# Kernel tuning notes

Measured on AMD Instinct MI355X. Metric: run time of the kernel, lower is better.

Reference implementation:

```python
import jax, jax.numpy as jnp
import numpy as np

D_MODEL = 1024

def setup_inputs() -> dict:
    key = jax.random.key(0)
    ks = jax.random.split(key, 5)
    s = 1.0 / np.sqrt(D_MODEL)  # torch Linear default init scale-ish
    x = jax.random.normal(ks[0], (4, 2048, D_MODEL), dtype=jnp.float32)
    Wq = jax.random.normal(ks[1], (D_MODEL, D_MODEL), dtype=jnp.float32) * s
    Wk = jax.random.normal(ks[2], (D_MODEL, D_MODEL), dtype=jnp.float32) * s
    Wv = jax.random.normal(ks[3], (D_MODEL, D_MODEL), dtype=jnp.float32) * s
    Wo = jax.random.normal(ks[4], (D_MODEL, D_MODEL), dtype=jnp.float32) * s
    z = jnp.zeros((D_MODEL,), dtype=jnp.float32)
    return {"x": x, "Wq": Wq, "bq": z, "Wk": Wk, "bk": z, "Wv": Wv, "bv": z, "Wo": Wo, "bo": z}

def reference(x, Wq, bq, Wk, bk, Wv, bv, Wo, bo):
    # x: (B, S, D). Single-head causal attention, dropout in eval mode (identity).
    B, S, D = x.shape
    Q = jnp.einsum('bsd,ed->bse', x, Wq) + bq
    K = jnp.einsum('bsd,ed->bse', x, Wk) + bk
    V = jnp.einsum('bsd,ed->bse', x, Wv) + bv
    scores = jnp.einsum('bqd,bkd->bqk', Q, K) / jnp.sqrt(jnp.float32(D))
    causal = jnp.tril(jnp.ones((S, S), dtype=bool))  # (S, S)
    scores = jnp.where(causal, scores, -jnp.inf)
    weights = jax.nn.softmax(scores, axis=-1)
    attended = jnp.einsum('bqk,bkd->bqd', weights, V)
    out = jnp.einsum('bsd,ed->bse', attended, Wo) + bo
    return out
```

## Files before the change

kernel.cpp:

```cpp
#include <hip/hip_runtime.h>
#include <cstdint>
#include <cstddef>


#define D_MODEL 1024
#define SEQ     2048
#define BATCH   4

typedef unsigned short u16;
typedef __bf16 bf16_t;
typedef bf16_t bf16x8 __attribute__((ext_vector_type(8)));
typedef float  f32x4  __attribute__((ext_vector_type(4)));
typedef u16    u16x4  __attribute__((ext_vector_type(4)));

__device__ __forceinline__ u16 f2bf(float x) {
  union { float f; uint32_t u; } v; v.f = x;
  uint32_t r = v.u + 0x7fffu + ((v.u >> 16) & 1u);
  return (u16)(r >> 16);
}
__device__ __forceinline__ float bf2f(u16 h) {
  union { uint32_t u; float f; } v; v.u = (uint32_t)h << 16;
  return v.f;
}

__device__ __forceinline__ void gload_lds16(const u16* g, u16* l) {
  __builtin_amdgcn_global_load_lds((__attribute__((address_space(1))) void*)g,
                                   (__attribute__((address_space(3))) void*)l,
                                   16, 0, 0);
}

__device__ __forceinline__ void gemm_core(const u16* __restrict__ Ablk,
                                          const u16* __restrict__ Bblk,
                                          int lda, int ldb, int ksteps32,
                                          u16* As, u16* Bs,
                                          f32x4 acc[4][4]) {
  const int tid  = threadIdx.x;
  const int lane = tid & 63;
  const int wave = tid >> 6;
  const int wr = (wave >> 1) * 64, wc = (wave & 1) * 64;
  const int frow = lane & 15, kc = lane >> 4;
  const int ch0 = tid, ch1 = 256 + tid;
  const int m0 = ch0 >> 2, k80 = (((ch0 & 3) ^ ((m0 >> 1) & 3))) * 8;
  const int m1 = ch1 >> 2, k81 = (((ch1 & 3) ^ ((m1 >> 1) & 3))) * 8;
  int aoff[4], boff[4];
#pragma unroll
  for (int i = 0; i < 4; ++i) {
    const int ra = wr + i * 16 + frow;
    aoff[i] = (ra * 4 + (kc ^ ((ra >> 1) & 3))) * 8;
    const int rb = wc + i * 16 + frow;
    boff[i] = (rb * 4 + (kc ^ ((rb >> 1) & 3))) * 8;
  }
  for (int kt = 0; kt < ksteps32; ++kt) {
    __syncthreads();
    const int kb = kt * 32;
    gload_lds16(Ablk + (size_t)m0 * lda + kb + k80, As + ch0 * 8);
    gload_lds16(Ablk + (size_t)m1 * lda + kb + k81, As + ch1 * 8);
    gload_lds16(Bblk + (size_t)m0 * ldb + kb + k80, Bs + ch0 * 8);
    gload_lds16(Bblk + (size_t)m1 * ldb + kb + k81, Bs + ch1 * 8);
    asm volatile("s_waitcnt vmcnt(0)" ::: "memory");
    __syncthreads();

    bf16x8 af[4], bf[4];
#pragma unroll
    for (int i = 0; i < 4; ++i) af[i] = *(const bf16x8*)(As + aoff[i]);
#pragma unroll
    for (int j = 0; j < 4; ++j) bf[j] = *(const bf16x8*)(Bs + boff[j]);
#pragma unroll
    for (int i = 0; i < 4; ++i)
#pragma unroll
      for (int j = 0; j < 4; ++j)
        acc[i][j] = __builtin_amdgcn_mfma_f32_16x16x32_bf16(af[i], bf[j], acc[i][j], 0, 0, 0);
  }
}

__global__ __launch_bounds__(256) void cvt_kernel(const float4* __restrict__ x,
                                                  const float4* __restrict__ wq,
                                                  const float4* __restrict__ wk,
                                                  const float4* __restrict__ wv,
                                                  const float4* __restrict__ wo,
                                                  u16* __restrict__ dst) {
  const int i = blockIdx.x * 256 + threadIdx.x;
  float4 v;
  if (i < 2097152) {
    v = x[i];
  } else {
    const int j = i - 2097152;
    const int w = j >> 18;
    const float4* s = (w == 0) ? wq : (w == 1) ? wk : (w == 2) ? wv : wo;
    v = s[j & 262143];
  }
  u16x4 o = {f2bf(v.x), f2bf(v.y), f2bf(v.z), f2bf(v.w)};
  *(u16x4*)(dst + (size_t)i * 4) = o;
}

__global__ void transposeW_kernel(const u16* __restrict__ src, u16* __restrict__ dst) {
  __shared__ u16 tile[32][33];
  const int r0 = blockIdx.x * 32, c0 = blockIdx.y * 32;
  const int tx = threadIdx.x, ty = threadIdx.y;
#pragma unroll
  for (int r = 0; r < 4; ++r)
    tile[ty + r * 8][tx] = src[(size_t)(r0 + ty + r * 8) * D_MODEL + c0 + tx];
  __syncthreads();
#pragma unroll
  for (int r = 0; r < 4; ++r)
    dst[(size_t)(c0 + ty + r * 8) * D_MODEL + r0 + tx] = tile[tx][ty + r * 8];
}

__global__ __launch_bounds__(256) void stageA_kernel(
    const u16* __restrict__ xb,
    const u16* __restrict__ WqB, const u16* __restrict__ WkB,
    const u16* __restrict__ WoB, const u16* __restrict__ WvT,
    const float* __restrict__ Wo32, const float* __restrict__ bv,
    const float* __restrict__ bq, const float* __restrict__ bk,
    u16* __restrict__ Qb, u16* __restrict__ Kb,
    u16* __restrict__ Wp, float* __restrict__ bp) {
  __shared__ __align__(16) u16 As[4096];
  __shared__ __align__(16) u16 Bs[4096];
  const int blk = blockIdx.x;
  const int lane = threadIdx.x & 63, wave = threadIdx.x >> 6;
  const int wr = (wave >> 1) * 64, wc = (wave & 1) * 64;
  const int cl = lane & 15, rl = (lane >> 4) * 4;

  if (blk < 64) {
    const int f0 = (blk >> 3) * 128, e0 = (blk & 7) * 128;
    f32x4 acc[4][4] = {};
    gemm_core(WoB + (size_t)f0 * D_MODEL, WvT + (size_t)e0 * D_MODEL,
              D_MODEL, D_MODEL, 32, As, Bs, acc);
#pragma unroll
    for (int j = 0; j < 4; ++j) {
      const int col = e0 + wc + j * 16 + cl;
#pragma unroll
      for (int i = 0; i < 4; ++i)
#pragma unroll
        for (int r = 0; r < 4; ++r) {
          const int row = f0 + wr + i * 16 + rl + r;
          Wp[(size_t)row * D_MODEL + col] = f2bf(acc[i][j][r]);
        }
    }
  } else if (blk < 80) {
    const int f = (blk - 64) * 64 + (threadIdx.x >> 2);
    const int dq = threadIdx.x & 3;
    const float* row = Wo32 + (size_t)f * D_MODEL + dq * 256;
    const float* bvq = bv + dq * 256;
    float s = 0.f;
#pragma unroll 8
    for (int i = 0; i < 256; ++i) s += row[i] * bvq[i];
    s += __shfl_xor(s, 1);
    s += __shfl_xor(s, 2);
    if (dq == 0) bp[f] = s;
  } else {
    const int v = blk - 80;
    const int c = v & 7, s = v >> 3;
    const int row0 = (c * 8 + (s >> 4)) * 128;
    const int cz = s & 15;
    const int z = cz >> 3;
    const int col0 = (cz & 7) * 128;
    const u16*   W    = z ? WkB : WqB;
    const float* bias = z ? bk : bq;
    u16*         out  = z ? Kb : Qb;
    f32x4 acc[4][4] = {};
    gemm_core(xb + (size_t)row0 * D_MODEL, W + (size_t)col0 * D_MODEL,
              D_MODEL, D_MODEL, 32, As, Bs, acc);
#pragma unroll
    for (int j = 0; j < 4; ++j) {
      const int col = col0 + wc + j * 16 + cl;
      const float bb = bias[col];
#pragma unroll
      for (int i = 0; i < 4; ++i)
#pragma unroll
        for (int r = 0; r < 4; ++r) {
          const int row = row0 + wr + i * 16 + rl + r;
          out[(size_t)row * D_MODEL + col] = f2bf(acc[i][j][r] + bb);
        }
    }
  }
}

__global__ __launch_bounds__(256) void stageB_kernel(
    const u16* __restrict__ xb, const u16* __restrict__ Wp,
    const float* __restrict__ bp,
    const u16* __restrict__ Qb, const u16* __restrict__ Kb,
    u16* __restrict__ Vt, u16* __restrict__ Eb, float* __restrict__ rssum) {
  __shared__ __align__(16) u16 As[4096];
  __shared__ __align__(16) u16 Bs[4096];
  const int blk = blockIdx.x;
  const int lane = threadIdx.x & 63, wave = threadIdx.x >> 6;
  const int wr = (wave >> 1) * 64, wc = (wave & 1) * 64;
  const int cl = lane & 15, rl = (lane >> 4) * 4;

  if (blk < 544) {
    const int c = blk & 7, s = blk >> 3;
    int b, qi, ji;
    if (s < 48) {
      static const int sq_tab[6] = {1, 2, 2, 3, 3, 3};
      static const int sj_tab[6] = {0, 0, 1, 0, 1, 2};
      const int fi = c * 3 + (s >> 4);
      const int off = s & 15;
      b = fi / 6;
      const int fs = fi % 6;
      qi = sq_tab[fs] * 4 + (off >> 2);
      ji = sj_tab[fs] * 4 + (off & 3);
    } else {
      static const int di_tab[10] = {0, 1, 1, 2, 2, 2, 3, 3, 3, 3};
      static const int dj_tab[10] = {0, 0, 1, 0, 1, 2, 0, 1, 2, 3};
      const int k = (s - 48) / 10;
      const int off = (s - 48) % 10;
      const int di = c * 2 + k;
      b = di >> 2;
      const int dk = di & 3;
      qi = dk * 4 + di_tab[off];
      ji = dk * 4 + dj_tab[off];
    }
    const u16* A  = Qb + (size_t)(b * SEQ + qi * 128) * D_MODEL;
    const u16* Bt = Kb + (size_t)(b * SEQ + ji * 128) * D_MODEL;
    f32x4 acc[4][4] = {};
    gemm_core(A, Bt, D_MODEL, D_MODEL, 32, As, Bs, acc);
    u16* out = Eb + (size_t)b * SEQ * SEQ;
    float* rs = rssum + b * SEQ;
#pragma unroll
    for (int i = 0; i < 4; ++i)
#pragma unroll
      for (int r = 0; r < 4; ++r) {
        const int q = qi * 128 + wr + i * 16 + rl + r;
        float ps = 0.f;
#pragma unroll
        for (int j = 0; j < 4; ++j) {
          const int jj = ji * 128 + wc + j * 16 + cl;
          u16 h16 = (jj <= q) ? f2bf(__expf(acc[i][j][r] * 0.03125f)) : (u16)0;
          out[(size_t)q * SEQ + jj] = h16;
          ps += bf2f(h16);
        }
        ps += __shfl_xor(ps, 1);
        ps += __shfl_xor(ps, 2);
        ps += __shfl_xor(ps, 4);
        ps += __shfl_xor(ps, 8);
        if (cl == 0) atomicAdd(&rs[q], ps);
      }
  } else {
    const int v = blk - 544;
    const int c = v & 7, s = v >> 3;
    const int row0 = (c * 8 + (s >> 3)) * 128;
    const int col0 = (s & 7) * 128;
    f32x4 acc[4][4] = {};
    gemm_core(xb + (size_t)row0 * D_MODEL, Wp + (size_t)col0 * D_MODEL,
              D_MODEL, D_MODEL, 32, As, Bs, acc);
    const int b = row0 >> 11;
    u16* vt = Vt + (size_t)b * D_MODEL * SEQ;
#pragma unroll
    for (int j = 0; j < 4; ++j) {
      const int col = col0 + wc + j * 16 + cl;
      const float bb = bp[col];
#pragma unroll
      for (int i = 0; i < 4; ++i) {
        const int s0 = (row0 & 2047) + wr + i * 16 + rl;
        u16x4 o = {f2bf(acc[i][j][0] + bb), f2bf(acc[i][j][1] + bb),
                   f2bf(acc[i][j][2] + bb), f2bf(acc[i][j][3] + bb)};
        *(u16x4*)(vt + (size_t)col * SEQ + s0) = o;
      }
    }
  }
}

__global__ __launch_bounds__(256) void pv_kernel(const u16* __restrict__ Eb,
                                                 const u16* __restrict__ Vt,
                                                 const float* __restrict__ rssum,
                                                 const float* __restrict__ bo,
                                                 float* __restrict__ Out) {
  __shared__ __align__(16) u16 As[4096];
  __shared__ __align__(16) u16 Bs[4096];
  const int blk = blockIdx.x;
  const int half = blk >> 8, idx = blk & 255;
  const int c = idx & 7, s = idx >> 3;
  const int b  = c >> 1;
  const int dt = (c & 1) * 4 + (s & 3);
  const int m  = s >> 2;
  const int qt = half ? (15 - 2 * m) : (2 * m);
  const u16* A  = Eb + (size_t)b * SEQ * SEQ + (size_t)(qt * 128) * SEQ;
  const u16* Bt = Vt + (size_t)b * D_MODEL * SEQ + (size_t)(dt * 128) * SEQ;
  f32x4 acc[4][4] = {};
  gemm_core(A, Bt, SEQ, SEQ, (qt + 1) * 4, As, Bs, acc);
  const int lane = threadIdx.x & 63, wave = threadIdx.x >> 6;
  const int wr = (wave >> 1) * 64, wc = (wave & 1) * 64;
  const int cl = lane & 15, rl = (lane >> 4) * 4;
#pragma unroll
  for (int i = 0; i < 4; ++i)
#pragma unroll
    for (int r = 0; r < 4; ++r) {
      const int row = qt * 128 + wr + i * 16 + rl + r;
      const float invl = 1.0f / rssum[b * SEQ + row];
#pragma unroll
      for (int j = 0; j < 4; ++j) {
        const int col = dt * 128 + wc + j * 16 + cl;
        Out[(size_t)(b * SEQ + row) * D_MODEL + col] = acc[i][j][r] * invl + bo[col];
      }
    }
}

extern "C" void kernel_launch(void* const* d_in, const int* in_sizes, int n_in,
                              void* d_out, int out_size, void* d_ws, size_t ws_size,
                              hipStream_t stream) {
  const float* x  = (const float*)d_in[0];
  const float* Wq = (const float*)d_in[1];
  const float* bq = (const float*)d_in[2];
  const float* Wk = (const float*)d_in[3];
  const float* bk = (const float*)d_in[4];
  const float* Wv = (const float*)d_in[5];
  const float* bv = (const float*)d_in[6];
  const float* Wo = (const float*)d_in[7];
  const float* bo = (const float*)d_in[8];
  float* out = (float*)d_out;
  char* ws = (char*)d_ws;

  u16*   xb  = (u16*)(ws);
  u16*   Wb  = (u16*)(ws + (16u << 20));
  u16*   Qb  = (u16*)(ws + (24u << 20));
  u16*   Kb  = (u16*)(ws + (40u << 20));
  u16*   Vt  = (u16*)(ws + (56u << 20));
  u16*   Eb  = (u16*)(ws + (72u << 20));
  u16*   WvT = (u16*)(ws + (104u << 20));
  u16*   Wp  = (u16*)(ws + (106u << 20));
  float* bp  = (float*)(ws + (108u << 20));
  float* rssum = (float*)(ws + (20u << 20));

  cvt_kernel<<<12288, 256, 0, stream>>>((const float4*)x, (const float4*)Wq,
                                        (const float4*)Wk, (const float4*)Wv,
                                        (const float4*)Wo, xb);
  transposeW_kernel<<<dim3(32, 32), dim3(32, 8), 0, stream>>>(Wb + (2u << 20), WvT);
  stageA_kernel<<<1104, 256, 0, stream>>>(xb, Wb, Wb + (1u << 20), Wb + (3u << 20),
                                          WvT, Wo, bv, bq, bk, Qb, Kb, Wp, bp);
  hipMemsetAsync(rssum, 0, BATCH * SEQ * sizeof(float), stream);
  stageB_kernel<<<1056, 256, 0, stream>>>(xb, Wp, bp, Qb, Kb, Vt, Eb, rssum);
  pv_kernel<<<512, 256, 0, stream>>>(Eb, Vt, rssum, bo, out);
}
```

Before: 267.3 us.

## Fuse convert, Wv transpose and rssum zeroing into one prep kernel; reorder PV tiles

Merges the fp32-to-bf16 conversion, the Wv transpose (now reading fp32 Wv directly and skipping the bf16 Wv copy) and the rssum memset into a single launch. This removes two launches, the memset, and a round trip through the bf16 Wv buffer. The PV kernel's block-to-tile mapping also changes from paired light/heavy query tiles to a heaviest-first descending order, to balance the causal workload. The tradeoff is that the conversion blocks now loop four times each, and the transpose reads uncoalesced-width fp32.

After: 265.5 us. No clear change (-0.7%).

```diff
diff --git a/kernel.cpp b/kernel.cpp
--- a/kernel.cpp
+++ b/kernel.cpp
@@ -73,37 +73,58 @@
   }
 }
 
-__global__ __launch_bounds__(256) void cvt_kernel(const float4* __restrict__ x,
-                                                  const float4* __restrict__ wq,
-                                                  const float4* __restrict__ wk,
-                                                  const float4* __restrict__ wv,
-                                                  const float4* __restrict__ wo,
-                                                  u16* __restrict__ dst) {
-  const int i = blockIdx.x * 256 + threadIdx.x;
-  float4 v;
-  if (i < 2097152) {
-    v = x[i];
+__global__ __launch_bounds__(256) void prep_kernel(const float4* __restrict__ x,
+                                                   const float4* __restrict__ wq,
+                                                   const float4* __restrict__ wk,
+                                                   const float4* __restrict__ wv,
+                                                   const float4* __restrict__ wo,
+                                                   const float* __restrict__ wv32,
+                                                   u16* __restrict__ dst,
+                                                   u16* __restrict__ wvt,
+                                                   float* __restrict__ rssum) {
+  const int blk = blockIdx.x, tid = threadIdx.x;
+  if (blk < 3072) {
+#pragma unroll
+    for (int g = 0; g < 4; ++g) {
+      const int i = (g * 3072 + blk) * 256 + tid;
+      float4 v;
+      bool store = true;
+      if (i < 2097152) {
+        v = x[i];
+      } else {
+        const int j = i - 2097152;
+        const int w = j >> 18;
+        if (w == 2) { store = false; }
+        else {
+          const float4* s = (w == 0) ? wq : (w == 1) ? wk : wo;
+          v = s[j & 262143];
+        }
+      }
+      if (store) {
+        u16x4 o = {f2bf(v.x), f2bf(v.y), f2bf(v.z), f2bf(v.w)};
+        *(u16x4*)(dst + (size_t)i * 4) = o;
+      }
+    }
+  } else if (blk < 4096) {
+    __shared__ u16 tile[32][33];
+    const int tb = blk - 3072;
+    const int r0 = (tb >> 5) * 32, c0 = (tb & 31) * 32;
+    const int tx = tid & 31, ty = tid >> 5;
+#pragma unroll
+    for (int r = 0; r < 4; ++r)
+      tile[ty + r * 8][tx] = f2bf(wv32[(size_t)(r0 + ty + r * 8) * D_MODEL + c0 + tx]);
+    __syncthreads();
+#pragma unroll
+    for (int r = 0; r < 4; ++r)
+      wvt[(size_t)(c0 + ty + r * 8) * D_MODEL + r0 + tx] = tile[tx][ty + r * 8];
   } else {
-    const int j = i - 2097152;
-    const int w = j >> 18;
-    const float4* s = (w == 0) ? wq : (w == 1) ? wk : (w == 2) ? wv : wo;
-    v = s[j & 262143];
-  }
-  u16x4 o = {f2bf(v.x), f2bf(v.y), f2bf(v.z), f2bf(v.w)};
-  *(u16x4*)(dst + (size_t)i * 4) = o;
-}
-
-__global__ void transposeW_kernel(const u16* __restrict__ src, u16* __restrict__ dst) {
-  __shared__ u16 tile[32][33];
-  const int r0 = blockIdx.x * 32, c0 = blockIdx.y * 32;
-  const int tx = threadIdx.x, ty = threadIdx.y;
-#pragma unroll
-  for (int r = 0; r < 4; ++r)
-    tile[ty + r * 8][tx] = src[(size_t)(r0 + ty + r * 8) * D_MODEL + c0 + tx];
-  __syncthreads();
-#pragma unroll
-  for (int r = 0; r < 4; ++r)
-    dst[(size_t)(c0 + ty + r * 8) * D_MODEL + r0 + tx] = tile[tx][ty + r * 8];
+    f32x4* p = (f32x4*)rssum;
+#pragma unroll
+    for (int k = 0; k < 8; ++k) {
+      f32x4 z = {0.f, 0.f, 0.f, 0.f};
+      p[k * 256 + tid] = z;
+    }
+  }
 }
 
 __global__ __launch_bounds__(256) void stageA_kernel(
@@ -268,13 +289,11 @@
                                                  float* __restrict__ Out) {
   __shared__ __align__(16) u16 As[4096];
   __shared__ __align__(16) u16 Bs[4096];
-  const int blk = blockIdx.x;
-  const int half = blk >> 8, idx = blk & 255;
-  const int c = idx & 7, s = idx >> 3;
+  const int u = blockIdx.x;
+  const int c = u & 7, s = u >> 3;
   const int b  = c >> 1;
-  const int dt = (c & 1) * 4 + (s & 3);
-  const int m  = s >> 2;
-  const int qt = half ? (15 - 2 * m) : (2 * m);
+  const int dt = (c & 1) * 4 + (s >> 4);
+  const int qt = 15 - (s & 15);
   const u16* A  = Eb + (size_t)b * SEQ * SEQ + (size_t)(qt * 128) * SEQ;
   const u16* Bt = Vt + (size_t)b * D_MODEL * SEQ + (size_t)(dt * 128) * SEQ;
   f32x4 acc[4][4] = {};
@@ -322,13 +341,11 @@
   float* bp  = (float*)(ws + (108u << 20));
   float* rssum = (float*)(ws + (20u << 20));
 
-  cvt_kernel<<<12288, 256, 0, stream>>>((const float4*)x, (const float4*)Wq,
+  prep_kernel<<<4097, 256, 0, stream>>>((const float4*)x, (const float4*)Wq,
                                         (const float4*)Wk, (const float4*)Wv,
-                                        (const float4*)Wo, xb);
-  transposeW_kernel<<<dim3(32, 32), dim3(32, 8), 0, stream>>>(Wb + (2u << 20), WvT);
+                                        (const float4*)Wo, Wv, xb, WvT, rssum);
   stageA_kernel<<<1104, 256, 0, stream>>>(xb, Wb, Wb + (1u << 20), Wb + (3u << 20),
                                           WvT, Wo, bv, bq, bk, Qb, Kb, Wp, bp);
-  hipMemsetAsync(rssum, 0, BATCH * SEQ * sizeof(float), stream);
   stageB_kernel<<<1056, 256, 0, stream>>>(xb, Wp, bp, Qb, Kb, Vt, Eb, rssum);
   pv_kernel<<<512, 256, 0, stream>>>(Eb, Vt, rssum, bo, out);
 }
```
